# Optimization experiments

Hardware: AMD Instinct MI355X
Metric: run time of the kernel (lower is better)

Reference implementation:

```python
import jax, jax.numpy as jnp
import numpy as np

D_MODEL = 1024
N_HEADS = 16
D_V = D_MODEL // N_HEADS  # 64; o_proj maps d_model -> d_v (quirk of the source)
B, S = 4, 2048


def setup_inputs() -> dict:
    key = jax.random.key(0)
    ks = jax.random.split(key, 5)
    scale = 1.0 / np.sqrt(D_MODEL)
    return {
        "in_features": jax.random.normal(ks[0], (B, S, D_MODEL), dtype=jnp.float32),
        "Wq": jax.random.normal(ks[1], (D_MODEL, D_MODEL), dtype=jnp.float32) * scale,
        "Wk": jax.random.normal(ks[2], (D_MODEL, D_MODEL), dtype=jnp.float32) * scale,
        "Wv": jax.random.normal(ks[3], (D_MODEL, D_MODEL), dtype=jnp.float32) * scale,
        "Wo": jax.random.normal(ks[4], (D_V, D_MODEL), dtype=jnp.float32) * scale,
    }


def reference(in_features, Wq, Wk, Wv, Wo):
    # Linear(in, out): y = x @ W^T, no bias. NOTE: source never splits heads;
    # attention runs single-head over the full d_model dims.
    Q = jnp.einsum('bsd,ed->bse', in_features, Wq)  # [B,S,D]
    K = jnp.einsum('bsd,ed->bse', in_features, Wk)
    V = jnp.einsum('bsd,ed->bse', in_features, Wv)

    scores = jnp.einsum('bqd,bkd->bqk', Q, K)       # [B,S,S]
    causal = jnp.tril(jnp.ones((S, S), dtype=bool))  # True = keep
    # source applies -inf mask BEFORE scaling (equivalent result)
    scores = jnp.where(causal[None, :, :], scores, -jnp.inf)
    scores = scores / jnp.sqrt(jnp.float32(D_MODEL))  # K.size(-1) == d_model
    attn = jax.nn.softmax(scores, axis=-1)
    ctx = jnp.einsum('bqk,bkd->bqd', attn, V)        # [B,S,D]
    return jnp.einsum('bsd,vd->bsv', ctx, Wo)        # [B,S,D_V]
```

## Files before the change

### kernel.cpp

```cpp
#include <hip/hip_runtime.h>
#include <math.h>

typedef unsigned short u16;
typedef unsigned int u32;
typedef __attribute__((ext_vector_type(8))) short short8;
typedef __attribute__((ext_vector_type(4))) short short4v;
typedef __attribute__((ext_vector_type(4))) float f32x4;

#define BB 4
#define SS 2048
#define DD 1024
#define DV 64
#define NYU 1152
#define BS (BB * SS)
#define SCALE (1.0f / 32.0f)

__device__ __forceinline__ u16 f2bf(float f) {
    u32 u = __builtin_bit_cast(u32, f);
    u32 r = u + 0x7fffu + ((u >> 16) & 1u);
    return (u16)(r >> 16);
}
__device__ __forceinline__ float bf2f(u16 b) {
    return __builtin_bit_cast(float, (u32)b << 16);
}
__device__ __forceinline__ void storeC(float* p, float v) { *p = v; }
__device__ __forceinline__ void storeC(u16* p, float v) { *p = f2bf(v); }

__global__ __launch_bounds__(256) void prep(const float* __restrict__ x,
                                            const float* __restrict__ Wq,
                                            const float* __restrict__ Wk,
                                            const float* __restrict__ Wo,
                                            const float* __restrict__ Wv,
                                            u16* __restrict__ x16,
                                            u16* __restrict__ Wqt,
                                            u16* __restrict__ Wkt,
                                            float* __restrict__ wpart,
                                            float* __restrict__ out,
                                            float* __restrict__ Lacc) {
    __shared__ float smem[64 * 128];
    const int b = blockIdx.x;
    const int tid = threadIdx.x;
    if (b < 8192) {
        int i = b * 256 + tid;
        f32x4 v = ((const f32x4*)x)[i];
        short4v o;
        o.x = (short)f2bf(v.x); o.y = (short)f2bf(v.y);
        o.z = (short)f2bf(v.z); o.w = (short)f2bf(v.w);
        ((short4v*)x16)[i] = o;
    } else if (b < 8704) {
        const int bb = b - 8192;
        const float* src = (bb >> 8) ? Wk : Wq;
        u16* dst = (bb >> 8) ? Wkt : Wqt;
        const int rem = bb & 255;
        const int e0 = (rem >> 4) * 64, d0 = (rem & 15) * 64;
        u16* t = (u16*)smem;
        const int g = tid >> 6, lane = tid & 63;
        for (int r = g; r < 64; r += 4)
            t[r * 72 + lane] = f2bf(src[(size_t)(e0 + r) * DD + d0 + lane]);
        __syncthreads();
        for (int r = g; r < 64; r += 4)
            dst[(size_t)(d0 + r) * DD + e0 + lane] = t[lane * 72 + r];
    } else if (b < 8768) {
        const int bb = b - 8704;
        const int echunk = (bb & 7) * 128;
        const int kc = bb >> 3, kbase = kc * 128;
        for (int idx = tid; idx < 64 * 128; idx += 256)
            smem[idx] = Wo[(size_t)(idx >> 7) * DD + kbase + (idx & 127)];
        __syncthreads();
        const int eo = echunk + (tid & 31) * 4;
        const int ob = (tid >> 5) * 8;
        float acc[8][4] = {};
        for (int k = 0; k < 128; ++k) {
            f32x4 wv = *(const f32x4*)&Wv[(size_t)(kbase + k) * DD + eo];
#pragma unroll
            for (int oi = 0; oi < 8; ++oi) {
                float s = smem[(ob + oi) * 128 + k];
                acc[oi][0] += s * wv.x; acc[oi][1] += s * wv.y;
                acc[oi][2] += s * wv.z; acc[oi][3] += s * wv.w;
            }
        }
#pragma unroll
        for (int oi = 0; oi < 8; ++oi)
            *(f32x4*)&wpart[((size_t)kc * 64 + ob + oi) * DD + eo] =
                (f32x4){acc[oi][0], acc[oi][1], acc[oi][2], acc[oi][3]};
    } else if (b < 9280) {
        int i = (b - 8768) * 256 + tid;
        ((f32x4*)out)[i] = (f32x4){0.f, 0.f, 0.f, 0.f};
    } else {
        int i = (b - 9280) * 256 + tid;
        ((f32x4*)Lacc)[i] = (f32x4){0.f, 0.f, 0.f, 0.f};
    }
}

__global__ __launch_bounds__(256) void reduce_all(const float* __restrict__ Gpart,
                                                  const float* __restrict__ wpart,
                                                  u16* __restrict__ Wall2) {
    const int bx = blockIdx.x;
    const int e0 = threadIdx.x * 4;
    f32x4 s = (f32x4){0.f, 0.f, 0.f, 0.f};
    if (bx < 1024) {
#pragma unroll
        for (int kc = 0; kc < 4; ++kc)
            s += *(const f32x4*)&Gpart[(size_t)kc * DD * DD + (size_t)bx * DD + e0];
    } else {
#pragma unroll
        for (int kc = 0; kc < 8; ++kc)
            s += *(const f32x4*)&wpart[((size_t)kc * 64 + bx - 1024) * DD + e0];
    }
    short4v ov;
    ov.x = (short)f2bf(s.x); ov.y = (short)f2bf(s.y);
    ov.z = (short)f2bf(s.z); ov.w = (short)f2bf(s.w);
    *(short4v*)&Wall2[(size_t)bx * DD + e0] = ov;
}

template <int TM, int TN, int WM, int WN, typename OutT, int MODE>
__global__ __launch_bounds__(WM * WN * 64) void gemm_nt_mfma(
    const u16* __restrict__ A, const u16* __restrict__ B, OutT* __restrict__ C,
    int lda, int ldb, int ldc, int K, long sA, long sB, long sC,
    u16* __restrict__ Utp) {
    constexpr int NW = WM * WN;
    constexpr int CA = TM / 16;
    constexpr int CB = TN / 16;

    const int z = blockIdx.z;
    A += (size_t)z * sA;
    B += (size_t)z * sB;
    C += (size_t)z * sC;
    int m0, n0;
    if constexpr (MODE == 3) {
        const int b = blockIdx.x;
        const int r = b & 7, q = b >> 3;
        m0 = (r * 8 + q / 9) * TM;
        n0 = (q % 9) * TN;
    } else {
        m0 = blockIdx.y * TM;
        n0 = blockIdx.x * TN;
    }

    __shared__ u16 As[TM * 32];
    __shared__ u16 Bs[TN * 32];

    const int tid = threadIdx.x;
    const int w = tid >> 6, lane = tid & 63;
    const int wm = w / WN, wn = w % WN;
    const int lrow = lane >> 2;
    const int lcol = (lane & 3) * 8;
    const int m16 = lane & 15;
    const int kh = (lane >> 4) * 8;

    f32x4 acc[4][4];
#pragma unroll
    for (int i = 0; i < 4; ++i)
#pragma unroll
        for (int j = 0; j < 4; ++j) acc[i][j] = (f32x4){0.f, 0.f, 0.f, 0.f};

    for (int k0 = 0; k0 < K; k0 += 32) {
        for (int c = w; c < CA; c += NW) {
            const u16* g = A + (size_t)(m0 + c * 16 + lrow) * lda + k0 + lcol;
            __builtin_amdgcn_global_load_lds(
                (const __attribute__((address_space(1))) void*)g,
                (__attribute__((address_space(3))) void*)(&As[c * 512]), 16, 0, 0);
        }
        for (int c = w; c < CB; c += NW) {
            const u16* g = B + (size_t)(n0 + c * 16 + lrow) * ldb + k0 + lcol;
            __builtin_amdgcn_global_load_lds(
                (const __attribute__((address_space(1))) void*)g,
                (__attribute__((address_space(3))) void*)(&Bs[c * 512]), 16, 0, 0);
        }
        __syncthreads();

        short8 a[4], b[4];
#pragma unroll
        for (int i = 0; i < 4; ++i)
            a[i] = *(const short8*)&As[(wm * 64 + i * 16 + m16) * 32 + kh];
#pragma unroll
        for (int j = 0; j < 4; ++j)
            b[j] = *(const short8*)&Bs[(wn * 64 + j * 16 + m16) * 32 + kh];
#pragma unroll
        for (int i = 0; i < 4; ++i)
#pragma unroll
            for (int j = 0; j < 4; ++j)
                acc[i][j] = __builtin_amdgcn_mfma_f32_16x16x32_bf16(a[i], b[j], acc[i][j], 0, 0, 0);
        __syncthreads();
    }

    const int crow0 = m0 + wm * 64 + (lane >> 4) * 4;
    const int ccol0 = n0 + wn * 64 + m16;
#pragma unroll
    for (int i = 0; i < 4; ++i)
#pragma unroll
        for (int j = 0; j < 4; ++j)
#pragma unroll
            for (int r = 0; r < 4; ++r) {
                const float v = acc[i][j][r];
                storeC(&C[(size_t)(crow0 + i * 16 + r) * ldc + ccol0 + j * 16], v);
                if constexpr (MODE == 3) {
                    if (n0 == 1024 && wn == 0)
                        Utp[(size_t)(ccol0 + j * 16 - 1024) * BS + crow0 + i * 16 + r] = f2bf(v);
                }
            }
}

__global__ __launch_bounds__(256) void scores_pv(const u16* __restrict__ YU,
                                                 const u16* __restrict__ x16,
                                                 const u16* __restrict__ Ut,
                                                 float* __restrict__ out,
                                                 float* __restrict__ Lacc) {
    const int b = blockIdx.x;
    const int r8 = b & 7;
    const int z = r8 >> 1;
    const int t = 2 * (b >> 3) + (r8 & 1);
    int y = (int)((sqrtf(8.f * t + 1.f) - 1.f) * 0.5f);
    while ((y + 1) * (y + 2) / 2 <= t) ++y;
    while (y * (y + 1) / 2 > t) --y;
    const int m0 = y * 128;
    const int n0 = (t - y * (y + 1) / 2) * 128;

    const u16* A = YU + (size_t)z * SS * NYU;
    const u16* B = x16 + (size_t)z * SS * DD;

    __shared__ union ShU {
        struct { u16 As[128 * 32]; u16 Bs[128 * 32]; } s;
        u16 Ps[128 * 136];
    } sh;

    const int tid = threadIdx.x;
    const int w = tid >> 6, lane = tid & 63;
    const int wm = w >> 1, wn = w & 1;
    const int lrow = lane >> 2;
    const int lcol = (lane & 3) * 8;
    const int m16 = lane & 15;
    const int kh = (lane >> 4) * 8;

    f32x4 acc[4][4];
#pragma unroll
    for (int i = 0; i < 4; ++i)
#pragma unroll
        for (int j = 0; j < 4; ++j) acc[i][j] = (f32x4){0.f, 0.f, 0.f, 0.f};

    for (int k0 = 0; k0 < DD; k0 += 32) {
        for (int c = w; c < 8; c += 4) {
            const u16* g = A + (size_t)(m0 + c * 16 + lrow) * NYU + k0 + lcol;
            __builtin_amdgcn_global_load_lds(
                (const __attribute__((address_space(1))) void*)g,
                (__attribute__((address_space(3))) void*)(&sh.s.As[c * 512]), 16, 0, 0);
        }
        for (int c = w; c < 8; c += 4) {
            const u16* g = B + (size_t)(n0 + c * 16 + lrow) * DD + k0 + lcol;
            __builtin_amdgcn_global_load_lds(
                (const __attribute__((address_space(1))) void*)g,
                (__attribute__((address_space(3))) void*)(&sh.s.Bs[c * 512]), 16, 0, 0);
        }
        __syncthreads();

        short8 a[4], bb[4];
#pragma unroll
        for (int i = 0; i < 4; ++i)
            a[i] = *(const short8*)&sh.s.As[(wm * 64 + i * 16 + m16) * 32 + kh];
#pragma unroll
        for (int j = 0; j < 4; ++j)
            bb[j] = *(const short8*)&sh.s.Bs[(wn * 64 + j * 16 + m16) * 32 + kh];
#pragma unroll
        for (int i = 0; i < 4; ++i)
#pragma unroll
            for (int j = 0; j < 4; ++j)
                acc[i][j] = __builtin_amdgcn_mfma_f32_16x16x32_bf16(a[i], bb[j], acc[i][j], 0, 0, 0);
        __syncthreads();
    }

    const int rl0 = wm * 64 + (lane >> 4) * 4;
    const int cl0 = wn * 64 + m16;
#pragma unroll
    for (int i = 0; i < 4; ++i)
#pragma unroll
        for (int j = 0; j < 4; ++j)
#pragma unroll
            for (int r = 0; r < 4; ++r) {
                const int rl = rl0 + i * 16 + r;
                const int cl = cl0 + j * 16;
                float p = __expf(acc[i][j][r] * SCALE);
                sh.Ps[rl * 136 + cl] = (n0 + cl <= m0 + rl) ? f2bf(p) : (u16)0;
            }
    __syncthreads();

    short8 ones8;
#pragma unroll
    for (int e = 0; e < 8; ++e) ones8[e] = (short)0x3F80;

    const u16* Utz = Ut + (size_t)z * SS + n0;
    f32x4 accO[2][4], accL[2];
#pragma unroll
    for (int i = 0; i < 2; ++i) {
        accL[i] = (f32x4){0.f, 0.f, 0.f, 0.f};
#pragma unroll
        for (int j = 0; j < 4; ++j) accO[i][j] = (f32x4){0.f, 0.f, 0.f, 0.f};
    }
#pragma unroll
    for (int ks = 0; ks < 4; ++ks) {
        const int k0 = ks * 32;
        short8 a[2], bb[4];
#pragma unroll
        for (int i = 0; i < 2; ++i)
            a[i] = *(const short8*)&sh.Ps[(w * 32 + i * 16 + m16) * 136 + k0 + kh];
#pragma unroll
        for (int j = 0; j < 4; ++j)
            bb[j] = *(const short8*)&Utz[(size_t)(j * 16 + m16) * BS + k0 + kh];
#pragma unroll
        for (int i = 0; i < 2; ++i) {
#pragma unroll
            for (int j = 0; j < 4; ++j)
                accO[i][j] = __builtin_amdgcn_mfma_f32_16x16x32_bf16(a[i], bb[j], accO[i][j], 0, 0, 0);
            accL[i] = __builtin_amdgcn_mfma_f32_16x16x32_bf16(a[i], ones8, accL[i], 0, 0, 0);
        }
    }

    float* Oz = out + (size_t)z * SS * DV;
    float* Lz = Lacc + (size_t)z * SS;
    const int wrow = m0 + w * 32 + (lane >> 4) * 4;
#pragma unroll
    for (int i = 0; i < 2; ++i) {
#pragma unroll
        for (int j = 0; j < 4; ++j)
#pragma unroll
            for (int r = 0; r < 4; ++r)
                atomicAdd(&Oz[(size_t)(wrow + i * 16 + r) * DV + j * 16 + m16],
                          accO[i][j][r]);
        if (m16 == 0)
#pragma unroll
            for (int r = 0; r < 4; ++r)
                atomicAdd(&Lz[wrow + i * 16 + r], accL[i][r]);
    }
}

__global__ __launch_bounds__(256) void normalize(float* __restrict__ out,
                                                 const float* __restrict__ Lacc) {
    int i = blockIdx.x * 256 + threadIdx.x;
    f32x4 v = ((f32x4*)out)[i];
    const float inv = 1.f / Lacc[(i * 4) >> 6];
    v.x *= inv; v.y *= inv; v.z *= inv; v.w *= inv;
    ((f32x4*)out)[i] = v;
}

extern "C" void kernel_launch(void* const* d_in, const int* in_sizes, int n_in,
                              void* d_out, int out_size, void* d_ws, size_t ws_size,
                              hipStream_t stream) {
    const float* x  = (const float*)d_in[0];
    const float* Wq = (const float*)d_in[1];
    const float* Wk = (const float*)d_in[2];
    const float* Wv = (const float*)d_in[3];
    const float* Wo = (const float*)d_in[4];
    float* out = (float*)d_out;

    u16* x16   = (u16*)d_ws;
    u16* Wqt16 = x16 + (size_t)BB * SS * DD;
    u16* Wkt16 = Wqt16 + (size_t)DD * DD;
    u16* Wall2 = Wkt16 + (size_t)DD * DD;
    u16* YU    = Wall2 + (size_t)NYU * DD;
    u16* Ut    = YU + (size_t)BB * SS * NYU;
    float* wpart = (float*)(Ut + (size_t)DV * BS);
    float* Lacc  = wpart + (size_t)8 * 64 * DD;
    float* Gpart = (float*)YU;

    prep<<<dim3(9288), 256, 0, stream>>>(x, Wq, Wk, Wo, Wv, x16, Wqt16, Wkt16,
                                         wpart, out, Lacc);

    gemm_nt_mfma<128, 128, 2, 2, float, 0><<<dim3(8, 8, 4), 256, 0, stream>>>(
        Wkt16, Wqt16, Gpart, DD, DD, DD, 256, 256, 256, (long)DD * DD, nullptr);

    reduce_all<<<dim3(1088), 256, 0, stream>>>(Gpart, wpart, Wall2);

    gemm_nt_mfma<128, 128, 2, 2, u16, 3><<<dim3(576), 256, 0, stream>>>(
        x16, Wall2, YU, DD, DD, NYU, DD, 0, 0, 0, Ut);

    scores_pv<<<dim3(544), 256, 0, stream>>>(YU, x16, Ut, out, Lacc);

    normalize<<<dim3(out_size / 4 / 256), 256, 0, stream>>>(out, Lacc);
}
```

Measured before the change: 205.3 us.

## Double-buffer LDS tiles and XOR-swizzle columns in GEMM and attention kernels

Both the generic GEMM kernel and the fused attention-score kernel now keep two LDS buffers for the A and B tiles. The next k-slice is prefetched with global_load_lds while the current slice feeds the MFMAs, which removes one barrier per iteration. The 16-byte column chunks are also XOR-swizzled by row, so the short8 LDS reads for MFMA operands hit fewer bank conflicts. LDS use doubles, which may lower occupancy, and the s_waitcnt vmcnt(0) placed before the barrier still exposes part of the load latency.

```diff
diff --git a/kernel.cpp b/kernel.cpp
--- a/kernel.cpp
+++ b/kernel.cpp
@@ -137,16 +137,17 @@
         n0 = blockIdx.x * TN;
     }
 
-    __shared__ u16 As[TM * 32];
-    __shared__ u16 Bs[TN * 32];
+    __shared__ u16 As[2][TM * 32];
+    __shared__ u16 Bs[2][TN * 32];
 
     const int tid = threadIdx.x;
     const int w = tid >> 6, lane = tid & 63;
     const int wm = w / WN, wn = w % WN;
     const int lrow = lane >> 2;
-    const int lcol = (lane & 3) * 8;
+    const int lcolsw = (((lane & 3) ^ ((lrow >> 1) & 3)) << 3);
     const int m16 = lane & 15;
-    const int kh = (lane >> 4) * 8;
+    const int khg = lane >> 4;
+    const int rdo = ((khg ^ ((m16 >> 1) & 3)) << 3);
 
     f32x4 acc[4][4];
 #pragma unroll
@@ -154,34 +155,43 @@
 #pragma unroll
         for (int j = 0; j < 4; ++j) acc[i][j] = (f32x4){0.f, 0.f, 0.f, 0.f};
 
-    for (int k0 = 0; k0 < K; k0 += 32) {
+    auto stage = [&](int t, int bufi) {
+        const int k0 = t * 32;
         for (int c = w; c < CA; c += NW) {
-            const u16* g = A + (size_t)(m0 + c * 16 + lrow) * lda + k0 + lcol;
+            const u16* g = A + (size_t)(m0 + c * 16 + lrow) * lda + k0 + lcolsw;
             __builtin_amdgcn_global_load_lds(
                 (const __attribute__((address_space(1))) void*)g,
-                (__attribute__((address_space(3))) void*)(&As[c * 512]), 16, 0, 0);
+                (__attribute__((address_space(3))) void*)(&As[bufi][c * 512]), 16, 0, 0);
         }
         for (int c = w; c < CB; c += NW) {
-            const u16* g = B + (size_t)(n0 + c * 16 + lrow) * ldb + k0 + lcol;
+            const u16* g = B + (size_t)(n0 + c * 16 + lrow) * ldb + k0 + lcolsw;
             __builtin_amdgcn_global_load_lds(
                 (const __attribute__((address_space(1))) void*)g,
-                (__attribute__((address_space(3))) void*)(&Bs[c * 512]), 16, 0, 0);
-        }
+                (__attribute__((address_space(3))) void*)(&Bs[bufi][c * 512]), 16, 0, 0);
+        }
+    };
+
+    const int nk = K >> 5;
+    stage(0, 0);
+    int cur = 0;
+    for (int t = 0; t < nk; ++t) {
+        asm volatile("s_waitcnt vmcnt(0)" ::: "memory");
         __syncthreads();
+        if (t + 1 < nk) stage(t + 1, cur ^ 1);
 
         short8 a[4], b[4];
 #pragma unroll
         for (int i = 0; i < 4; ++i)
-            a[i] = *(const short8*)&As[(wm * 64 + i * 16 + m16) * 32 + kh];
-#pragma unroll
-        for (int j = 0; j < 4; ++j)
-            b[j] = *(const short8*)&Bs[(wn * 64 + j * 16 + m16) * 32 + kh];
+            a[i] = *(const short8*)&As[cur][(wm * 64 + i * 16 + m16) * 32 + rdo];
+#pragma unroll
+        for (int j = 0; j < 4; ++j)
+            b[j] = *(const short8*)&Bs[cur][(wn * 64 + j * 16 + m16) * 32 + rdo];
 #pragma unroll
         for (int i = 0; i < 4; ++i)
 #pragma unroll
             for (int j = 0; j < 4; ++j)
                 acc[i][j] = __builtin_amdgcn_mfma_f32_16x16x32_bf16(a[i], b[j], acc[i][j], 0, 0, 0);
-        __syncthreads();
+        cur ^= 1;
     }
 
     const int crow0 = m0 + wm * 64 + (lane >> 4) * 4;
@@ -220,7 +230,7 @@
     const u16* B = x16 + (size_t)z * SS * DD;
 
     __shared__ union ShU {
-        struct { u16 As[128 * 32]; u16 Bs[128 * 32]; } s;
+        struct { u16 As[2][128 * 32]; u16 Bs[2][128 * 32]; } s;
         u16 Ps[128 * 136];
     } sh;
 
@@ -228,9 +238,10 @@
     const int w = tid >> 6, lane = tid & 63;
     const int wm = w >> 1, wn = w & 1;
     const int lrow = lane >> 2;
-    const int lcol = (lane & 3) * 8;
+    const int lcolsw = (((lane & 3) ^ ((lrow >> 1) & 3)) << 3);
     const int m16 = lane & 15;
     const int kh = (lane >> 4) * 8;
+    const int rdo = (((lane >> 4) ^ ((m16 >> 1) & 3)) << 3);
 
     f32x4 acc[4][4];
 #pragma unroll
@@ -238,35 +249,44 @@
 #pragma unroll
         for (int j = 0; j < 4; ++j) acc[i][j] = (f32x4){0.f, 0.f, 0.f, 0.f};
 
-    for (int k0 = 0; k0 < DD; k0 += 32) {
+    auto stage = [&](int tt, int bufi) {
+        const int k0 = tt * 32;
         for (int c = w; c < 8; c += 4) {
-            const u16* g = A + (size_t)(m0 + c * 16 + lrow) * NYU + k0 + lcol;
+            const u16* g = A + (size_t)(m0 + c * 16 + lrow) * NYU + k0 + lcolsw;
             __builtin_amdgcn_global_load_lds(
                 (const __attribute__((address_space(1))) void*)g,
-                (__attribute__((address_space(3))) void*)(&sh.s.As[c * 512]), 16, 0, 0);
+                (__attribute__((address_space(3))) void*)(&sh.s.As[bufi][c * 512]), 16, 0, 0);
         }
         for (int c = w; c < 8; c += 4) {
-            const u16* g = B + (size_t)(n0 + c * 16 + lrow) * DD + k0 + lcol;
+            const u16* g = B + (size_t)(n0 + c * 16 + lrow) * DD + k0 + lcolsw;
             __builtin_amdgcn_global_load_lds(
                 (const __attribute__((address_space(1))) void*)g,
-                (__attribute__((address_space(3))) void*)(&sh.s.Bs[c * 512]), 16, 0, 0);
-        }
+                (__attribute__((address_space(3))) void*)(&sh.s.Bs[bufi][c * 512]), 16, 0, 0);
+        }
+    };
+
+    stage(0, 0);
+    int cur = 0;
+    for (int tt = 0; tt < 32; ++tt) {
+        asm volatile("s_waitcnt vmcnt(0)" ::: "memory");
         __syncthreads();
+        if (tt + 1 < 32) stage(tt + 1, cur ^ 1);
 
         short8 a[4], bb[4];
 #pragma unroll
         for (int i = 0; i < 4; ++i)
-            a[i] = *(const short8*)&sh.s.As[(wm * 64 + i * 16 + m16) * 32 + kh];
-#pragma unroll
-        for (int j = 0; j < 4; ++j)
-            bb[j] = *(const short8*)&sh.s.Bs[(wn * 64 + j * 16 + m16) * 32 + kh];
+            a[i] = *(const short8*)&sh.s.As[cur][(wm * 64 + i * 16 + m16) * 32 + rdo];
+#pragma unroll
+        for (int j = 0; j < 4; ++j)
+            bb[j] = *(const short8*)&sh.s.Bs[cur][(wn * 64 + j * 16 + m16) * 32 + rdo];
 #pragma unroll
         for (int i = 0; i < 4; ++i)
 #pragma unroll
             for (int j = 0; j < 4; ++j)
                 acc[i][j] = __builtin_amdgcn_mfma_f32_16x16x32_bf16(a[i], bb[j], acc[i][j], 0, 0, 0);
-        __syncthreads();
-    }
+        cur ^= 1;
+    }
+    __syncthreads();
 
     const int rl0 = wm * 64 + (lane >> 4) * 4;
     const int cl0 = wn * 64 + m16;
```

After: 200.2 us. 1.03x faster.
